# Optimization experiments

Hardware: AMD Instinct MI355X
Metric: run time of the kernel (lower is better)

Reference implementation:

```python
import jax, jax.numpy as jnp
import numpy as np

B, D, UNITS, T, M = 16384, 256, 256, 32, 64


def hard_sigmoid(x):
    # keras hard_sigmoid: clip(0.2*x + 0.5, 0, 1)
    return jnp.clip(0.2 * x + 0.5, 0.0, 1.0)


def setup_inputs() -> dict:
    key = jax.random.key(0)
    ks = jax.random.split(key, 11)
    inputs = jax.random.normal(ks[0], (B, D), jnp.float32)
    h_tm1 = jax.random.normal(ks[1], (B, UNITS), jnp.float32)
    c_tm1 = jax.random.normal(ks[2], (B, UNITS), jnp.float32)
    h_tm2 = jax.random.normal(ks[3], (B, UNITS), jnp.float32)
    c_tm2 = jax.random.normal(ks[4], (B, UNITS), jnp.float32)
    neighbors = jax.random.randint(ks[5], (B, T, M), 0, 2, jnp.int32)      # binary adjacency rows
    mapping = jax.random.randint(ks[6], (B, M), 0, T, jnp.int32)           # processing time of each node
    reverse_mapping = jax.random.randint(ks[7], (B, T), 0, T, jnp.int32)   # time -> row index in neighbors
    W = jax.random.normal(ks[8], (D, 4 * UNITS), jnp.float32) * 0.05
    U = jax.random.normal(ks[9], (UNITS, 4 * UNITS), jnp.float32) * 0.05
    Un = jax.random.normal(ks[10], (UNITS, 4 * UNITS), jnp.float32) * 0.05
    # unit_forget_bias: zeros for i, ones for f, zeros for c and o
    bias = jnp.concatenate([jnp.zeros((UNITS,)), jnp.ones((UNITS,)), jnp.zeros((2 * UNITS,))]).astype(jnp.float32)
    return {"inputs": inputs, "h_tm1": h_tm1, "c_tm1": c_tm1, "h_tm2": h_tm2, "c_tm2": c_tm2,
            "neighbors": neighbors, "mapping": mapping, "reverse_mapping": reverse_mapping,
            "time": 16, "W": W, "U": U, "Un": Un, "bias": bias}


def reference(inputs, h_tm1, c_tm1, h_tm2, c_tm2, neighbors, mapping, reverse_mapping, time, W, U, Un, bias):
    # --- neighbor row gather: ng_rows[b] = neighbors[b, reverse_mapping[b, time]] ---
    prev_pos = reverse_mapping[:, time]                                      # [B]
    ng_rows = jnp.take_along_axis(neighbors, prev_pos[:, None, None], axis=1)[:, 0, :]  # [B, M]
    ng_f = ng_rows.astype(jnp.float32)
    is_past = (mapping < time).astype(jnp.float32)                           # [B, M]
    ng_num = jnp.sum(ng_f, axis=-1)                                          # [B]
    cnt_past = jnp.sum(ng_f * is_past, axis=-1)                              # [B]
    cnt_fut = ng_num - cnt_past                                              # [B]
    denom = jnp.where(ng_num > 0, ng_num, 1.0)
    has_ng = (ng_num > 0)[:, None]

    # original sums the FULL-batch state for each neighbor (K.sum over axes [0,1]),
    # so aggregation collapses to count_past*sum(h_tm1) + count_fut*sum(h_tm2), div_no_nan by ng_num.
    hs1 = jnp.sum(h_tm1, axis=0)                                             # [units]
    hs2 = jnp.sum(h_tm2, axis=0)
    ngs = jnp.where(has_ng,
                    (cnt_past[:, None] * hs1[None, :] + cnt_fut[:, None] * hs2[None, :]) / denom[:, None],
                    0.0)                                                     # [B, units]

    # --- gates (implementation=1, no dropout) ---
    z_x = inputs @ W + bias                                                  # [B, 4*units]
    x_i, x_f, x_c, x_o = jnp.split(z_x, 4, axis=-1)                          # x_f_avg == x_f in source
    U_i, U_f, U_c, U_o = jnp.split(U, 4, axis=-1)
    Un_i, Un_f, Un_c, Un_o = jnp.split(Un, 4, axis=-1)

    i = hard_sigmoid(x_i + h_tm1 @ U_i + ngs @ Un_i)
    f_avg = hard_sigmoid(x_f + h_tm1 @ Un_f)   # note: uses Un_f per source
    f = hard_sigmoid(x_f + h_tm1 @ U_f)
    c = jnp.tanh(x_c + h_tm1 @ U_c + ngs @ Un_c)
    o = hard_sigmoid(x_o + h_tm1 @ U_o + ngs @ Un_o)

    # --- neighbor memory aggregation: same batch-summed structure with f_avg*c ---
    m1 = jnp.sum(f_avg * c_tm1, axis=0)                                      # [units]
    m2 = jnp.sum(f_avg * c_tm2, axis=0)
    mem_agg = jnp.where(has_ng,
                        (cnt_past[:, None] * m1[None, :] + cnt_fut[:, None] * m2[None, :]) / denom[:, None],
                        0.0)                                                 # [B, units]

    memory = mem_agg + f * c_tm1 + i * c
    h = o * jnp.tanh(memory)
    return h, memory
```

## Files before the change

kernel.cpp:

```cpp
#include <hip/hip_runtime.h>
#include <cmath>

#define BB 16384
#define DD 256
#define UU 256
#define TT 32
#define MM 64

#define WS_ALPHA 0
#define WS_BETA  16384
#define WS_M1    32768
#define WS_M2    33024
#define WS_V1    33280
#define WS_V2    34304
#define WS_PART1 35328
#define WS_PART2 68096
#define WS_BF16_BYTE 403456

typedef short bf16x8 __attribute__((ext_vector_type(8)));
typedef float f32x4  __attribute__((ext_vector_type(4)));

__device__ __forceinline__ float hsig(float x) {
    return fminf(1.0f, fmaxf(0.0f, fmaf(0.2f, x, 0.5f)));
}
__device__ __forceinline__ short f2bf(float x) {
    unsigned u = __float_as_uint(x);
    unsigned r = (u + 0x7fffu + ((u >> 16) & 1u)) >> 16;
    return (short)r;
}
__device__ __forceinline__ float bf2f(short h) {
    return __uint_as_float(((unsigned)(unsigned short)h) << 16);
}

__global__ void k_prep(const float* __restrict__ inputs, const float* __restrict__ h1,
                       const float* __restrict__ h2,
                       const int* __restrict__ neighbors, const int* __restrict__ mapping,
                       const int* __restrict__ revmap, const int* __restrict__ timep,
                       const float* __restrict__ W, const float* __restrict__ U,
                       const float* __restrict__ Un,
                       short* __restrict__ Ahi, short* __restrict__ Alo,
                       short* __restrict__ Bg,
                       float* __restrict__ alpha, float* __restrict__ beta,
                       float* __restrict__ part1, float* __restrict__ part2) {
    int blk = blockIdx.x;
    int tid = threadIdx.x;
    if (blk < 4096) {
        int q = tid & 3;
        int m = (blk & 255) * 64 + (tid >> 2);
        int kc = blk >> 8;
        int k0 = kc * 32 + q * 4;
        const float* src = (k0 < 256) ? (inputs + m * 256 + k0) : (h1 + m * 256 + k0 - 256);
        float4 x0 = *(const float4*)(src);
        float4 x1 = *(const float4*)(src + 16);
        float xs[8] = {x0.x, x0.y, x0.z, x0.w, x1.x, x1.y, x1.z, x1.w};
        bf16x8 hv, lv;
        #pragma unroll
        for (int j = 0; j < 8; j++) {
            short h = f2bf(xs[j]);
            hv[j] = h;
            lv[j] = f2bf(xs[j] - bf2f(h));
        }
        long doff = ((long)kc * 16384 + m) * 32 + q * 8;
        *(bf16x8*)(Ahi + doff) = hv;
        *(bf16x8*)(Alo + doff) = lv;
    } else if (blk < 4416) {
        int t = (blk - 4096) * 256 + tid;
        int q = t & 3;
        int r = t >> 2;
        int nl = r % 160;
        int r2 = r / 160;
        int kc = r2 & 15;
        int nb = r2 >> 4;
        int n = nb * 160 + nl;
        int g = (n >> 4) % 5;
        int u = (n / 80) * 16 + (n & 15);
        int c = (g < 4) ? g * 256 + u : 256 + u;
        bf16x8 hv, lv;
        #pragma unroll
        for (int j = 0; j < 8; j++) {
            int kl = q * 4 + (j & 3) + ((j >> 2) << 4);
            int k = kc * 32 + kl;
            const float* s;
            if (k < 256) s = W + k * 1024 + c;
            else         s = ((g < 4) ? U : Un) + (k - 256) * 1024 + c;
            float x = *s;
            short h = f2bf(x);
            hv[j] = h;
            lv[j] = f2bf(x - bf2f(h));
        }
        int off = (((nl * 64 + q * 16) ^ ((nl & 7) << 4)) >> 1);
        short* dst = Bg + (long)(nb * 16 + kc) * 10240 + off;
        *(bf16x8*)dst = hv;
        *(bf16x8*)(dst + 5120) = lv;
    } else if (blk < 8512) {
        int lane = tid & 63;
        int wid  = tid >> 6;
        int b = (blk - 4416) * 4 + wid;
        int t = timep[0];
        int p = revmap[b * TT + t];
        int ng = neighbors[(b * TT + p) * MM + lane];
        int mp = mapping[b * MM + lane];
        int cnt = ng;
        int cp  = (mp < t) ? ng : 0;
        #pragma unroll
        for (int off = 32; off > 0; off >>= 1) {
            cnt += __shfl_xor(cnt, off);
            cp  += __shfl_xor(cp, off);
        }
        if (lane == 0) {
            float a = 0.f, be = 0.f;
            if (cnt > 0) {
                float inv = 1.0f / (float)cnt;
                a  = (float)cp * inv;
                be = (float)(cnt - cp) * inv;
            }
            alpha[b] = a;
            beta[b]  = be;
        }
    } else {
        int p = blk - 8512;
        int r0 = p * 128;
        float s1 = 0.f, s2 = 0.f;
        for (int r = 0; r < 128; r++) {
            s1 += h1[(r0 + r) * UU + tid];
            s2 += h2[(r0 + r) * UU + tid];
        }
        part1[p * 256 + tid] = s1;
        part2[p * 256 + tid] = s2;
    }
}

__global__ void k_mid(const float* __restrict__ Un,
                      const float* __restrict__ part1, const float* __restrict__ part2,
                      float* __restrict__ v1, float* __restrict__ v2,
                      float* __restrict__ m12) {
    __shared__ float sh1[256], sh2[256];
    int tid = threadIdx.x;
    if (blockIdx.x == 0 && tid < 512) m12[tid] = 0.f;
    float s1 = 0.f, s2 = 0.f;
    #pragma unroll 8
    for (int p = 0; p < 128; p++) {
        s1 += part1[p * 256 + tid];
        s2 += part2[p * 256 + tid];
    }
    sh1[tid] = s1;
    sh2[tid] = s2;
    __syncthreads();
    int j = blockIdx.x * 256 + tid;
    float a1 = 0.f, a2 = 0.f;
    for (int k = 0; k < 256; k++) {
        float w = Un[k * 1024 + j];
        a1 = fmaf(sh1[k], w, a1);
        a2 = fmaf(sh2[k], w, a2);
    }
    v1[j] = a1;
    v2[j] = a2;
}

#define STAGE_B(KC, BUF) { \
    const char* _s = (const char*)(Bt + (long)(KC) * 10240); \
    char* _d = (char*)(&Bs[BUF][0]); \
    _Pragma("unroll") \
    for (int _c = 0; _c < 5; _c++) { \
        int _u = wv * 5120 + _c * 1024; \
        __builtin_amdgcn_global_load_lds( \
            (const __attribute__((address_space(1))) void*)(_s + _u + lane * 16), \
            (__attribute__((address_space(3))) void*)(_d + _u), 16, 0, 0); \
    } }

__global__ __launch_bounds__(256) void k_gemm_mfma(
    const short* __restrict__ Ahi, const short* __restrict__ Alo,
    const short* __restrict__ Bg,
    const float* __restrict__ c1p, const float* __restrict__ c2p,
    const float* __restrict__ bias,
    const float* __restrict__ alpha, const float* __restrict__ beta,
    const float* __restrict__ v1, const float* __restrict__ v2,
    float* __restrict__ m1, float* __restrict__ m2,
    float* __restrict__ out_h, float* __restrict__ out_mem)
{
    __shared__ short Bs[2][10240];

    const int tid = threadIdx.x;
    const int lane = tid & 63;
    const int wv = tid >> 6;
    const int mb = blockIdx.x;
    const int nb = blockIdx.y;
    const int m0 = mb * 128;
    const short* Bt = Bg + (long)nb * 163840;

    const int uloc = lane & 15;
    const int rgrp = lane >> 4;
    const int aoff = (m0 + wv * 32 + uloc) * 32 + rgrp * 8;
    const int bbase = ((uloc * 64 + rgrp * 16) ^ ((lane & 7) << 4));

    f32x4 acc[2][10];
    #pragma unroll
    for (int i = 0; i < 2; i++)
        #pragma unroll
        for (int j = 0; j < 10; j++) acc[i][j] = (f32x4){0.f, 0.f, 0.f, 0.f};

    STAGE_B(0, 0);
    bf16x8 ah0 = *(const bf16x8*)(Ahi + aoff);
    bf16x8 ah1 = *(const bf16x8*)(Ahi + aoff + 512);
    bf16x8 al0 = *(const bf16x8*)(Alo + aoff);
    bf16x8 al1 = *(const bf16x8*)(Alo + aoff + 512);

    for (int kc = 0; kc < 16; kc++) {
        __syncthreads();
        bf16x8 nh0, nh1, nl0, nl1;
        if (kc + 1 < 16) {
            STAGE_B(kc + 1, (kc + 1) & 1);
            long ab = (long)(kc + 1) * 524288 + aoff;
            nh0 = *(const bf16x8*)(Ahi + ab);
            nh1 = *(const bf16x8*)(Ahi + ab + 512);
            nl0 = *(const bf16x8*)(Alo + ab);
            nl1 = *(const bf16x8*)(Alo + ab + 512);
        }

        const char* bp = (const char*)Bs + (kc & 1) * 20480 + bbase;
        #pragma unroll
        for (int nf = 0; nf < 10; nf++) {
            bf16x8 bh = *(const bf16x8*)(bp + nf * 1024);
            bf16x8 bl = *(const bf16x8*)(bp + 10240 + nf * 1024);
            acc[0][nf] = __builtin_amdgcn_mfma_f32_16x16x32_bf16(ah0, bh, acc[0][nf], 0, 0, 0);
            acc[1][nf] = __builtin_amdgcn_mfma_f32_16x16x32_bf16(ah1, bh, acc[1][nf], 0, 0, 0);
            acc[0][nf] = __builtin_amdgcn_mfma_f32_16x16x32_bf16(al0, bh, acc[0][nf], 0, 0, 0);
            acc[1][nf] = __builtin_amdgcn_mfma_f32_16x16x32_bf16(al1, bh, acc[1][nf], 0, 0, 0);
            acc[0][nf] = __builtin_amdgcn_mfma_f32_16x16x32_bf16(ah0, bl, acc[0][nf], 0, 0, 0);
            acc[1][nf] = __builtin_amdgcn_mfma_f32_16x16x32_bf16(ah1, bl, acc[1][nf], 0, 0, 0);
        }
        if (kc + 1 < 16) { ah0 = nh0; ah1 = nh1; al0 = nl0; al1 = nl1; }
    }

    float pm1[2] = {0.f, 0.f}, pm2[2] = {0.f, 0.f};
    #pragma unroll
    for (int ub = 0; ub < 2; ub++) {
        int u = nb * 32 + ub * 16 + uloc;
        float bi = bias[u], bfv = bias[256 + u], bc = bias[512 + u], bo = bias[768 + u];
        float v1i = v1[u], v1c = v1[512 + u], v1o = v1[768 + u];
        float v2i = v2[u], v2c = v2[512 + u], v2o = v2[768 + u];
        #pragma unroll
        for (int mf = 0; mf < 2; mf++) {
            int bb = m0 + wv * 32 + mf * 16 + rgrp * 4;
            f32x4 fi = acc[mf][ub * 5 + 0];
            f32x4 ff = acc[mf][ub * 5 + 1];
            f32x4 fc = acc[mf][ub * 5 + 2];
            f32x4 fo = acc[mf][ub * 5 + 3];
            f32x4 fa = acc[mf][ub * 5 + 4];
            #pragma unroll
            for (int r = 0; r < 4; r++) {
                int b = bb + r;
                float al = alpha[b], be = beta[b];
                float c1 = c1p[b * 256 + u];
                float c2 = c2p[b * 256 + u];
                float zi  = fi[r] + bi + al * v1i + be * v2i;
                float zf  = ff[r] + bfv;
                float zc  = fc[r] + bc + al * v1c + be * v2c;
                float zo  = fo[r] + bo + al * v1o + be * v2o;
                float zfa = fa[r] + bfv;
                float ig = hsig(zi), fg = hsig(zf), og = hsig(zo), fav = hsig(zfa);
                float cg = tanhf(zc);
                out_mem[b * 256 + u] = fg * c1 + ig * cg;
                out_h[b * 256 + u]  = og;
                pm1[ub] += fav * c1;
                pm2[ub] += fav * c2;
            }
        }
    }

    #pragma unroll
    for (int ub = 0; ub < 2; ub++) {
        pm1[ub] += __shfl_xor(pm1[ub], 16); pm1[ub] += __shfl_xor(pm1[ub], 32);
        pm2[ub] += __shfl_xor(pm2[ub], 16); pm2[ub] += __shfl_xor(pm2[ub], 32);
    }
    __syncthreads();
    float* red = (float*)&Bs[0][0];
    if (rgrp == 0) {
        #pragma unroll
        for (int ub = 0; ub < 2; ub++) {
            red[((wv * 2 + 0) * 2 + ub) * 16 + uloc] = pm1[ub];
            red[((wv * 2 + 1) * 2 + ub) * 16 + uloc] = pm2[ub];
        }
    }
    __syncthreads();
    if (tid < 64) {
        int d = tid >> 5, ub = (tid >> 4) & 1, ui = tid & 15;
        float s = 0.f;
        #pragma unroll
        for (int w = 0; w < 4; w++) s += red[((w * 2 + d) * 2 + ub) * 16 + ui];
        atomicAdd(((d == 0) ? m1 : m2) + nb * 32 + ub * 16 + ui, s);
    }
}

__global__ void k_final(const float* __restrict__ alpha, const float* __restrict__ beta,
                        const float* __restrict__ m1, const float* __restrict__ m2,
                        float* __restrict__ out_h, float* __restrict__ out_mem) {
    int idx = blockIdx.x * 256 + threadIdx.x;
    int b  = idx >> 6;
    int uv = idx & 63;
    float4 mp = ((const float4*)out_mem)[idx];
    float4 ov = ((const float4*)out_h)[idx];
    float al = alpha[b], be = beta[b];
    float4 m1v = ((const float4*)m1)[uv];
    float4 m2v = ((const float4*)m2)[uv];
    float4 mem, h;
    mem.x = fmaf(al, m1v.x, fmaf(be, m2v.x, mp.x)); h.x = ov.x * tanhf(mem.x);
    mem.y = fmaf(al, m1v.y, fmaf(be, m2v.y, mp.y)); h.y = ov.y * tanhf(mem.y);
    mem.z = fmaf(al, m1v.z, fmaf(be, m2v.z, mp.z)); h.z = ov.z * tanhf(mem.z);
    mem.w = fmaf(al, m1v.w, fmaf(be, m2v.w, mp.w)); h.w = ov.w * tanhf(mem.w);
    ((float4*)out_mem)[idx] = mem;
    ((float4*)out_h)[idx]   = h;
}

extern "C" void kernel_launch(void* const* d_in, const int* in_sizes, int n_in,
                              void* d_out, int out_size, void* d_ws, size_t ws_size,
                              hipStream_t stream) {
    const float* inputs   = (const float*)d_in[0];
    const float* h_tm1    = (const float*)d_in[1];
    const float* c_tm1    = (const float*)d_in[2];
    const float* h_tm2    = (const float*)d_in[3];
    const float* c_tm2    = (const float*)d_in[4];
    const int*   neighbors= (const int*)d_in[5];
    const int*   mapping  = (const int*)d_in[6];
    const int*   revmap   = (const int*)d_in[7];
    const int*   timep    = (const int*)d_in[8];
    const float* W        = (const float*)d_in[9];
    const float* Uw       = (const float*)d_in[10];
    const float* Un       = (const float*)d_in[11];
    const float* bias     = (const float*)d_in[12];

    float* ws    = (float*)d_ws;
    float* alpha = ws + WS_ALPHA;
    float* beta  = ws + WS_BETA;
    float* m1    = ws + WS_M1;
    float* m2    = ws + WS_M2;
    float* v1    = ws + WS_V1;
    float* v2    = ws + WS_V2;
    float* part1 = ws + WS_PART1;
    float* part2 = ws + WS_PART2;

    short* Ahi = (short*)((char*)d_ws + WS_BF16_BYTE);
    short* Alo = Ahi + 8388608;
    short* Bg  = Alo + 8388608;

    float* out_h   = (float*)d_out;
    float* out_mem = out_h + BB * UU;

    k_prep<<<8640, 256, 0, stream>>>(inputs, h_tm1, h_tm2, neighbors, mapping, revmap,
                                     timep, W, Uw, Un, Ahi, Alo, Bg, alpha, beta,
                                     part1, part2);
    k_mid<<<4, 256, 0, stream>>>(Un, part1, part2, v1, v2, m1);

    dim3 g3(128, 8);
    k_gemm_mfma<<<g3, 256, 0, stream>>>(Ahi, Alo, Bg, c_tm1, c_tm2, bias,
                                        alpha, beta, v1, v2, m1, m2, out_h, out_mem);

    k_final<<<BB * UU / 4 / 256, 256, 0, stream>>>(alpha, beta, m1, m2, out_h, out_mem);
}
```

Measured before the change: 358.5 us.

## Switch GEMM to 32x32x16 MFMA with matching A/B packing layouts

Replaces the 16x16x32 bf16 MFMA tiling (2x10 fragments per wave) with 32x32x16 MFMA (5 gate accumulators of 16 floats each). The A and B prep packing is reordered to match the new operand layout, the B tile drops its XOR swizzle, and the epilogue and reduction are remapped to the 32-column accumulator layout. The larger MFMA is meant to cut instruction count and LDS operand reads per flop. The unswizzled LDS B reads could cause bank conflicts, and the per-lane row mapping changes how the epilogue's global memory accesses coalesce.

```diff
diff --git a/kernel.cpp b/kernel.cpp
--- a/kernel.cpp
+++ b/kernel.cpp
@@ -18,7 +18,7 @@
 #define WS_BF16_BYTE 403456
 
 typedef short bf16x8 __attribute__((ext_vector_type(8)));
-typedef float f32x4  __attribute__((ext_vector_type(4)));
+typedef float f32x16 __attribute__((ext_vector_type(16)));
 
 __device__ __forceinline__ float hsig(float x) {
     return fminf(1.0f, fmaxf(0.0f, fmaf(0.2f, x, 0.5f)));
@@ -48,48 +48,46 @@
         int q = tid & 3;
         int m = (blk & 255) * 64 + (tid >> 2);
         int kc = blk >> 8;
-        int k0 = kc * 32 + q * 4;
+        int s = q >> 1, h = q & 1;
+        int k0 = kc * 32 + s * 16 + h * 4;
         const float* src = (k0 < 256) ? (inputs + m * 256 + k0) : (h1 + m * 256 + k0 - 256);
         float4 x0 = *(const float4*)(src);
-        float4 x1 = *(const float4*)(src + 16);
+        float4 x1 = *(const float4*)(src + 8);
         float xs[8] = {x0.x, x0.y, x0.z, x0.w, x1.x, x1.y, x1.z, x1.w};
         bf16x8 hv, lv;
         #pragma unroll
         for (int j = 0; j < 8; j++) {
-            short h = f2bf(xs[j]);
-            hv[j] = h;
-            lv[j] = f2bf(xs[j] - bf2f(h));
+            short hh = f2bf(xs[j]);
+            hv[j] = hh;
+            lv[j] = f2bf(xs[j] - bf2f(hh));
         }
         long doff = ((long)kc * 16384 + m) * 32 + q * 8;
         *(bf16x8*)(Ahi + doff) = hv;
         *(bf16x8*)(Alo + doff) = lv;
     } else if (blk < 4416) {
         int t = (blk - 4096) * 256 + tid;
-        int q = t & 3;
-        int r = t >> 2;
-        int nl = r % 160;
-        int r2 = r / 160;
-        int kc = r2 & 15;
-        int nb = r2 >> 4;
-        int n = nb * 160 + nl;
-        int g = (n >> 4) % 5;
-        int u = (n / 80) * 16 + (n & 15);
+        int lane = t & 63;
+        int rest = t >> 6;
+        int gs = rest % 10;
+        int img = rest / 10;
+        int g = gs >> 1, s = gs & 1;
+        int nb = img >> 4, kc = img & 15;
+        int u = nb * 32 + (lane & 31);
+        int hl = lane >> 5;
         int c = (g < 4) ? g * 256 + u : 256 + u;
         bf16x8 hv, lv;
         #pragma unroll
         for (int j = 0; j < 8; j++) {
-            int kl = q * 4 + (j & 3) + ((j >> 2) << 4);
-            int k = kc * 32 + kl;
-            const float* s;
-            if (k < 256) s = W + k * 1024 + c;
-            else         s = ((g < 4) ? U : Un) + (k - 256) * 1024 + c;
-            float x = *s;
-            short h = f2bf(x);
-            hv[j] = h;
-            lv[j] = f2bf(x - bf2f(h));
-        }
-        int off = (((nl * 64 + q * 16) ^ ((nl & 7) << 4)) >> 1);
-        short* dst = Bg + (long)(nb * 16 + kc) * 10240 + off;
+            int k = kc * 32 + s * 16 + hl * 4 + (j & 3) + 8 * (j >> 2);
+            const float* sp;
+            if (k < 256) sp = W + k * 1024 + c;
+            else         sp = ((g < 4) ? U : Un) + (k - 256) * 1024 + c;
+            float x = *sp;
+            short hh = f2bf(x);
+            hv[j] = hh;
+            lv[j] = f2bf(x - bf2f(hh));
+        }
+        short* dst = Bg + (long)img * 10240 + gs * 512 + lane * 8;
         *(bf16x8*)dst = hv;
         *(bf16x8*)(dst + 5120) = lv;
     } else if (blk < 8512) {
@@ -188,107 +186,93 @@
     const int m0 = mb * 128;
     const short* Bt = Bg + (long)nb * 163840;
 
-    const int uloc = lane & 15;
-    const int rgrp = lane >> 4;
-    const int aoff = (m0 + wv * 32 + uloc) * 32 + rgrp * 8;
-    const int bbase = ((uloc * 64 + rgrp * 16) ^ ((lane & 7) << 4));
-
-    f32x4 acc[2][10];
+    const int col = lane & 31;
+    const int hl = lane >> 5;
+    const int m = m0 + wv * 32 + col;
+    const long abase = (long)m * 32 + hl * 8;
+
+    f32x16 acc[5];
     #pragma unroll
-    for (int i = 0; i < 2; i++)
-        #pragma unroll
-        for (int j = 0; j < 10; j++) acc[i][j] = (f32x4){0.f, 0.f, 0.f, 0.f};
+    for (int g = 0; g < 5; g++)
+        #pragma unroll
+        for (int r = 0; r < 16; r++) acc[g][r] = 0.f;
 
     STAGE_B(0, 0);
-    bf16x8 ah0 = *(const bf16x8*)(Ahi + aoff);
-    bf16x8 ah1 = *(const bf16x8*)(Ahi + aoff + 512);
-    bf16x8 al0 = *(const bf16x8*)(Alo + aoff);
-    bf16x8 al1 = *(const bf16x8*)(Alo + aoff + 512);
+    bf16x8 ah0 = *(const bf16x8*)(Ahi + abase);
+    bf16x8 ah1 = *(const bf16x8*)(Ahi + abase + 16);
+    bf16x8 al0 = *(const bf16x8*)(Alo + abase);
+    bf16x8 al1 = *(const bf16x8*)(Alo + abase + 16);
 
     for (int kc = 0; kc < 16; kc++) {
         __syncthreads();
         bf16x8 nh0, nh1, nl0, nl1;
         if (kc + 1 < 16) {
             STAGE_B(kc + 1, (kc + 1) & 1);
-            long ab = (long)(kc + 1) * 524288 + aoff;
+            long ab = abase + (long)(kc + 1) * 524288;
             nh0 = *(const bf16x8*)(Ahi + ab);
-            nh1 = *(const bf16x8*)(Ahi + ab + 512);
+            nh1 = *(const bf16x8*)(Ahi + ab + 16);
             nl0 = *(const bf16x8*)(Alo + ab);
-            nl1 = *(const bf16x8*)(Alo + ab + 512);
-        }
-
-        const char* bp = (const char*)Bs + (kc & 1) * 20480 + bbase;
-        #pragma unroll
-        for (int nf = 0; nf < 10; nf++) {
-            bf16x8 bh = *(const bf16x8*)(bp + nf * 1024);
-            bf16x8 bl = *(const bf16x8*)(bp + 10240 + nf * 1024);
-            acc[0][nf] = __builtin_amdgcn_mfma_f32_16x16x32_bf16(ah0, bh, acc[0][nf], 0, 0, 0);
-            acc[1][nf] = __builtin_amdgcn_mfma_f32_16x16x32_bf16(ah1, bh, acc[1][nf], 0, 0, 0);
-            acc[0][nf] = __builtin_amdgcn_mfma_f32_16x16x32_bf16(al0, bh, acc[0][nf], 0, 0, 0);
-            acc[1][nf] = __builtin_amdgcn_mfma_f32_16x16x32_bf16(al1, bh, acc[1][nf], 0, 0, 0);
-            acc[0][nf] = __builtin_amdgcn_mfma_f32_16x16x32_bf16(ah0, bl, acc[0][nf], 0, 0, 0);
-            acc[1][nf] = __builtin_amdgcn_mfma_f32_16x16x32_bf16(ah1, bl, acc[1][nf], 0, 0, 0);
+            nl1 = *(const bf16x8*)(Alo + ab + 16);
+        }
+
+        const char* bp = (const char*)Bs + (kc & 1) * 20480 + lane * 16;
+        #pragma unroll
+        for (int g = 0; g < 5; g++) {
+            bf16x8 bh0 = *(const bf16x8*)(bp + (g * 2 + 0) * 1024);
+            bf16x8 bh1 = *(const bf16x8*)(bp + (g * 2 + 1) * 1024);
+            bf16x8 bl0 = *(const bf16x8*)(bp + 10240 + (g * 2 + 0) * 1024);
+            bf16x8 bl1 = *(const bf16x8*)(bp + 10240 + (g * 2 + 1) * 1024);
+            acc[g] = __builtin_amdgcn_mfma_f32_32x32x16_bf16(ah0, bh0, acc[g], 0, 0, 0);
+            acc[g] = __builtin_amdgcn_mfma_f32_32x32x16_bf16(ah1, bh1, acc[g], 0, 0, 0);
+            acc[g] = __builtin_amdgcn_mfma_f32_32x32x16_bf16(al0, bh0, acc[g], 0, 0, 0);
+            acc[g] = __builtin_amdgcn_mfma_f32_32x32x16_bf16(al1, bh1, acc[g], 0, 0, 0);
+            acc[g] = __builtin_amdgcn_mfma_f32_32x32x16_bf16(ah0, bl0, acc[g], 0, 0, 0);
+            acc[g] = __builtin_amdgcn_mfma_f32_32x32x16_bf16(ah1, bl1, acc[g], 0, 0, 0);
         }
         if (kc + 1 < 16) { ah0 = nh0; ah1 = nh1; al0 = nl0; al1 = nl1; }
     }
 
-    float pm1[2] = {0.f, 0.f}, pm2[2] = {0.f, 0.f};
+    int u = nb * 32 + col;
+    float bi = bias[u], bfv = bias[256 + u], bc = bias[512 + u], bo = bias[768 + u];
+    float v1i = v1[u], v1c = v1[512 + u], v1o = v1[768 + u];
+    float v2i = v2[u], v2c = v2[512 + u], v2o = v2[768 + u];
+
+    float pm1 = 0.f, pm2 = 0.f;
     #pragma unroll
-    for (int ub = 0; ub < 2; ub++) {
-        int u = nb * 32 + ub * 16 + uloc;
-        float bi = bias[u], bfv = bias[256 + u], bc = bias[512 + u], bo = bias[768 + u];
-        float v1i = v1[u], v1c = v1[512 + u], v1o = v1[768 + u];
-        float v2i = v2[u], v2c = v2[512 + u], v2o = v2[768 + u];
-        #pragma unroll
-        for (int mf = 0; mf < 2; mf++) {
-            int bb = m0 + wv * 32 + mf * 16 + rgrp * 4;
-            f32x4 fi = acc[mf][ub * 5 + 0];
-            f32x4 ff = acc[mf][ub * 5 + 1];
-            f32x4 fc = acc[mf][ub * 5 + 2];
-            f32x4 fo = acc[mf][ub * 5 + 3];
-            f32x4 fa = acc[mf][ub * 5 + 4];
-            #pragma unroll
-            for (int r = 0; r < 4; r++) {
-                int b = bb + r;
-                float al = alpha[b], be = beta[b];
-                float c1 = c1p[b * 256 + u];
-                float c2 = c2p[b * 256 + u];
-                float zi  = fi[r] + bi + al * v1i + be * v2i;
-                float zf  = ff[r] + bfv;
-                float zc  = fc[r] + bc + al * v1c + be * v2c;
-                float zo  = fo[r] + bo + al * v1o + be * v2o;
-                float zfa = fa[r] + bfv;
-                float ig = hsig(zi), fg = hsig(zf), og = hsig(zo), fav = hsig(zfa);
-                float cg = tanhf(zc);
-                out_mem[b * 256 + u] = fg * c1 + ig * cg;
-                out_h[b * 256 + u]  = og;
-                pm1[ub] += fav * c1;
-                pm2[ub] += fav * c2;
-            }
-        }
-    }
-
-    #pragma unroll
-    for (int ub = 0; ub < 2; ub++) {
-        pm1[ub] += __shfl_xor(pm1[ub], 16); pm1[ub] += __shfl_xor(pm1[ub], 32);
-        pm2[ub] += __shfl_xor(pm2[ub], 16); pm2[ub] += __shfl_xor(pm2[ub], 32);
-    }
+    for (int r = 0; r < 16; r++) {
+        int row = (r & 3) + 8 * (r >> 2) + 4 * hl;
+        int b = m0 + wv * 32 + row;
+        float al = alpha[b], be = beta[b];
+        float c1 = c1p[b * 256 + u];
+        float c2 = c2p[b * 256 + u];
+        float zi  = acc[0][r] + bi + al * v1i + be * v2i;
+        float zf  = acc[1][r] + bfv;
+        float zc  = acc[2][r] + bc + al * v1c + be * v2c;
+        float zo  = acc[3][r] + bo + al * v1o + be * v2o;
+        float zfa = acc[4][r] + bfv;
+        float ig = hsig(zi), fg = hsig(zf), og = hsig(zo), fav = hsig(zfa);
+        float cg = tanhf(zc);
+        out_mem[b * 256 + u] = fg * c1 + ig * cg;
+        out_h[b * 256 + u]  = og;
+        pm1 += fav * c1;
+        pm2 += fav * c2;
+    }
+
+    pm1 += __shfl_xor(pm1, 32);
+    pm2 += __shfl_xor(pm2, 32);
     __syncthreads();
     float* red = (float*)&Bs[0][0];
-    if (rgrp == 0) {
-        #pragma unroll
-        for (int ub = 0; ub < 2; ub++) {
-            red[((wv * 2 + 0) * 2 + ub) * 16 + uloc] = pm1[ub];
-            red[((wv * 2 + 1) * 2 + ub) * 16 + uloc] = pm2[ub];
-        }
+    if (hl == 0) {
+        red[(wv * 2 + 0) * 32 + col] = pm1;
+        red[(wv * 2 + 1) * 32 + col] = pm2;
     }
     __syncthreads();
     if (tid < 64) {
-        int d = tid >> 5, ub = (tid >> 4) & 1, ui = tid & 15;
+        int d = tid >> 5, ui = tid & 31;
         float s = 0.f;
         #pragma unroll
-        for (int w = 0; w < 4; w++) s += red[((w * 2 + d) * 2 + ub) * 16 + ui];
-        atomicAdd(((d == 0) ? m1 : m2) + nb * 32 + ub * 16 + ui, s);
+        for (int w = 0; w < 4; w++) s += red[(w * 2 + d) * 32 + ui];
+        atomicAdd(((d == 0) ? m1 : m2) + nb * 32 + ui, s);
     }
 }
 
```

After: 361.7 us. Within noise of the previous version (+0.9%).
